# Kernel tuning notes

Measured on AMD Instinct MI355X. Metric: run time of the kernel, lower is better.

Reference implementation:

```python
import jax, jax.numpy as jnp
import numpy as np

B, C, F, D = 128, 16, 128, 512


def setup_inputs() -> dict:
    key = jax.random.key(0)
    k1, k2 = jax.random.split(key)
    return {
        "c_feats": jax.random.normal(k1, (B, C, D), dtype=jnp.float32),
        "f_feats": jax.random.normal(k2, (B, F, D), dtype=jnp.float32),
    }


def _dtw_path_masks(S):
    """S: [P, c, f] per-pair similarity. Returns [P, c, f] 0/1 max-path masks.

    DP: D[i,j] = max(D[i-1,j], D[i,j-1], D[i-1,j-1]) + S[i-1,j-1], D[0,0]=0,
    borders -inf. Tie-break priority (up, left, diag) matches Python max().
    Row recurrence is vectorized: D[i,j] = Csum[j] + cummax_k<=j(A[k]-Csum[k-1])
    where A[k]=max(D[i-1,k], D[i-1,k-1]) (wavefront-free row-parallel form).
    """
    P_, c, f = S.shape
    NEG = -jnp.inf

    init = jnp.concatenate([jnp.zeros((P_, 1), S.dtype),
                            jnp.full((P_, f), NEG, S.dtype)], axis=1)  # D[0, 0..f]

    def row_step(prev, dt_row):
        # prev: [P, f+1] = D[i-1, 0..f]; dt_row: [P, f] = S[i-1, :]
        A = jnp.maximum(prev[:, 1:], prev[:, :-1])                  # max(D[i-1,j], D[i-1,j-1])
        Ccum = jnp.cumsum(dt_row, axis=1)
        Cm1 = jnp.concatenate([jnp.zeros((P_, 1), dt_row.dtype), Ccum[:, :-1]], axis=1)
        row = Ccum + jax.lax.cummax(A - Cm1, axis=1)                # D[i, 1..f]
        new_prev = jnp.concatenate([jnp.full((P_, 1), NEG, dt_row.dtype), row], axis=1)
        return new_prev, new_prev

    _, rows = jax.lax.scan(row_step, init, jnp.moveaxis(S, 1, 0))   # [c, P, f+1]
    Dm = jnp.moveaxis(jnp.concatenate([init[None], rows], axis=0), 1, 0)  # [P, c+1, f+1]

    # Predecessor choice per cell; argmax picks first max -> priority up,left,diag
    up = Dm[:, :-1, 1:]
    left = Dm[:, 1:, :-1]
    diag = Dm[:, :-1, :-1]
    mv = jnp.argmax(jnp.stack([up, left, diag], axis=-1), axis=-1).astype(jnp.int32)
    mv = jnp.pad(mv, ((0, 0), (1, 0), (1, 0)))                      # [P, c+1, f+1]

    pidx = jnp.arange(P_)

    def bt_step(carry, _):
        mask, i, j = carry
        active = (i > 0) | (j > 0)
        mask = mask.at[pidx, i - 1, j - 1].add(jnp.where(active, 1.0, 0.0).astype(mask.dtype))
        m = mv[pidx, i, j]
        di = jnp.where(m == 1, 0, 1)   # left keeps i
        dj = jnp.where(m == 0, 0, 1)   # up keeps j
        i = jnp.where(active, i - di, i)
        j = jnp.where(active, j - dj, j)
        return (mask, i, j), None

    mask0 = jnp.zeros((P_, c, f), jnp.float32)
    i0 = jnp.full((P_,), c, jnp.int32)
    j0 = jnp.full((P_,), f, jnp.int32)
    (mask, _, _), _ = jax.lax.scan(bt_step, (mask0, i0, j0), None, length=c + f)
    return mask


def reference(c_feats, f_feats):
    b, c, d = c_feats.shape
    f = f_feats.shape[1]
    xn = c_feats / jnp.linalg.norm(c_feats, axis=-1, keepdims=True)
    yn = f_feats / jnp.linalg.norm(f_feats, axis=-1, keepdims=True)
    # Source quirk: y row j is normalized only once outer index i reaches it
    # (y[i-1] bug), so S[i,j] uses normalized y[j] iff j <= i, raw y[j] otherwise.
    Sn = jnp.einsum('mcd,nfd->mncf', xn, yn)
    Sr = jnp.einsum('mcd,nfd->mncf', xn, f_feats)
    tri = jnp.arange(f)[None, :] <= jnp.arange(c)[:, None]          # [c, f]: j <= i
    S = jnp.where(tri, Sn, Sr).reshape(b * b, c, f)
    return _dtw_path_masks(S).reshape(b, b, c, f)
```

## Files before the change

kernel.cpp:

```cpp
#include <hip/hip_runtime.h>
#include <stdint.h>

#define M_TOT 2048
#define N_TOT 16384
#define K_TOT 512

typedef _Float16 f16x8 __attribute__((ext_vector_type(8)));
typedef float f32x4 __attribute__((ext_vector_type(4)));
typedef float f32x16 __attribute__((ext_vector_type(16)));

#define AS1 __attribute__((address_space(1)))
#define AS3 __attribute__((address_space(3)))

__device__ __forceinline__ void ld_lds16(const void* g, void* l) {
    __builtin_amdgcn_global_load_lds((const AS1 void*)g, (AS3 void*)l, 16, 0, 0);
}

__device__ __forceinline__ void split4(float x0, float x1, float x2, float x3,
                                       uint2* hs, uint2* ls) {
    union U { _Float16 h[4]; uint2 u; } H, L;
    _Float16 h0 = (_Float16)x0; H.h[0] = h0; L.h[0] = (_Float16)(x0 - (float)h0);
    _Float16 h1 = (_Float16)x1; H.h[1] = h1; L.h[1] = (_Float16)(x1 - (float)h1);
    _Float16 h2 = (_Float16)x2; H.h[2] = h2; L.h[2] = (_Float16)(x2 - (float)h2);
    _Float16 h3 = (_Float16)x3; H.h[3] = h3; L.h[3] = (_Float16)(x3 - (float)h3);
    *hs = H.u; *ls = L.u;
}

__global__ __launch_bounds__(256) void norm_split_kernel(
    const float* __restrict__ c_feats, const float* __restrict__ f_feats,
    _Float16* __restrict__ Ah, _Float16* __restrict__ Al,
    _Float16* __restrict__ Bh, _Float16* __restrict__ Bl,
    float* __restrict__ normf)
{
    int wave = blockIdx.x * 4 + (threadIdx.x >> 6);
    int lane = threadIdx.x & 63;
    if (wave < 2048) {
        const float* row = c_feats + (size_t)wave * K_TOT;
        float4 v0 = ((const float4*)row)[lane];
        float4 v1 = ((const float4*)row)[lane + 64];
        double ss = (double)v0.x * v0.x + (double)v0.y * v0.y +
                    (double)v0.z * v0.z + (double)v0.w * v0.w +
                    (double)v1.x * v1.x + (double)v1.y * v1.y +
                    (double)v1.z * v1.z + (double)v1.w * v1.w;
        #pragma unroll
        for (int off = 32; off; off >>= 1) ss += __shfl_down(ss, off);
        double tot = __shfl(ss, 0);
        float nrm = sqrtf((float)tot);
        float a0 = v0.x / nrm, a1 = v0.y / nrm, a2 = v0.z / nrm, a3 = v0.w / nrm;
        float b0 = v1.x / nrm, b1 = v1.y / nrm, b2 = v1.z / nrm, b3 = v1.w / nrm;
        uint2 h, l;
        split4(a0, a1, a2, a3, &h, &l);
        ((uint2*)(Ah + (size_t)wave * K_TOT))[lane] = h;
        ((uint2*)(Al + (size_t)wave * K_TOT))[lane] = l;
        split4(b0, b1, b2, b3, &h, &l);
        ((uint2*)(Ah + (size_t)wave * K_TOT))[lane + 64] = h;
        ((uint2*)(Al + (size_t)wave * K_TOT))[lane + 64] = l;
    } else if (wave < 18432) {
        int fr = wave - 2048;
        const float* row = f_feats + (size_t)fr * K_TOT;
        float4 v0 = ((const float4*)row)[lane];
        float4 v1 = ((const float4*)row)[lane + 64];
        double ss = (double)v0.x * v0.x + (double)v0.y * v0.y +
                    (double)v0.z * v0.z + (double)v0.w * v0.w +
                    (double)v1.x * v1.x + (double)v1.y * v1.y +
                    (double)v1.z * v1.z + (double)v1.w * v1.w;
        #pragma unroll
        for (int off = 32; off; off >>= 1) ss += __shfl_down(ss, off);
        if (lane == 0) normf[fr] = sqrtf((float)ss);
        uint2 h, l;
        split4(v0.x, v0.y, v0.z, v0.w, &h, &l);
        ((uint2*)(Bh + (size_t)fr * K_TOT))[lane] = h;
        ((uint2*)(Bl + (size_t)fr * K_TOT))[lane] = l;
        split4(v1.x, v1.y, v1.z, v1.w, &h, &l);
        ((uint2*)(Bh + (size_t)fr * K_TOT))[lane + 64] = h;
        ((uint2*)(Bl + (size_t)fr * K_TOT))[lane + 64] = l;
    }
}

__global__ __launch_bounds__(256, 4) void mfma_gemm_kernel(
    const _Float16* __restrict__ Ah, const _Float16* __restrict__ Al,
    const _Float16* __restrict__ Bh, const _Float16* __restrict__ Bl,
    const float* __restrict__ normf,
    float* __restrict__ out)
{
    __shared__ _Float16 sAh[128 * 32];
    __shared__ _Float16 sAl[128 * 32];
    __shared__ _Float16 sBh[128 * 32];
    __shared__ _Float16 sBl[128 * 32];

    const int t = threadIdx.x;
    const int w = t >> 6, lane = t & 63;
    const int ntile = ((blockIdx.x & 7) << 4) | (blockIdx.x >> 3);
    const int gm0 = blockIdx.y * 128, gn0 = ntile * 128;
    const int wm = (w & 1) * 64, wn = (w >> 1) * 64;
    const int m32 = lane & 31;
    const int kql0 = lane >> 5;

    f32x16 acc[2][2] = {};
    const int l0 = w * 128 + lane;

    for (int k0 = 0; k0 < K_TOT; k0 += 32) {
        #pragma unroll
        for (int c = 0; c < 2; ++c) {
            int l = l0 + c * 64;
            int lrow = l >> 2, kq = l & 3;
            int kqs = kq ^ ((lrow >> 1) & 3);
            size_t goffA = (size_t)(gm0 + lrow) * K_TOT + k0 + kqs * 8;
            size_t goffB = (size_t)(gn0 + lrow) * K_TOT + k0 + kqs * 8;
            ld_lds16(Ah + goffA, sAh + (size_t)l * 8);
            ld_lds16(Al + goffA, sAl + (size_t)l * 8);
            ld_lds16(Bh + goffB, sBh + (size_t)l * 8);
            ld_lds16(Bl + goffB, sBl + (size_t)l * 8);
        }
        __syncthreads();

        #pragma unroll
        for (int kh = 0; kh < 2; ++kh) {
            f16x8 fah[2], fal[2], fbh[2], fbl[2];
            #pragma unroll
            for (int x = 0; x < 2; ++x) {
                int arr = wm + x * 32 + m32;
                int brr = wn + x * 32 + m32;
                int kqa = (kh * 2 + kql0) ^ ((arr >> 1) & 3);
                int kqb = (kh * 2 + kql0) ^ ((brr >> 1) & 3);
                int ar = arr * 32 + kqa * 8;
                int br = brr * 32 + kqb * 8;
                fah[x] = *(const f16x8*)(sAh + ar);
                fal[x] = *(const f16x8*)(sAl + ar);
                fbh[x] = *(const f16x8*)(sBh + br);
                fbl[x] = *(const f16x8*)(sBl + br);
            }
            #pragma unroll
            for (int mi = 0; mi < 2; ++mi)
                #pragma unroll
                for (int ni = 0; ni < 2; ++ni) {
                    acc[mi][ni] = __builtin_amdgcn_mfma_f32_32x32x16_f16(fah[mi], fbl[ni], acc[mi][ni], 0, 0, 0);
                    acc[mi][ni] = __builtin_amdgcn_mfma_f32_32x32x16_f16(fal[mi], fbh[ni], acc[mi][ni], 0, 0, 0);
                    acc[mi][ni] = __builtin_amdgcn_mfma_f32_32x32x16_f16(fah[mi], fbh[ni], acc[mi][ni], 0, 0, 0);
                }
        }
        __syncthreads();
    }

    const int nn = ntile;
    const int rq = 4 * (lane >> 5);
    #pragma unroll
    for (int ni = 0; ni < 2; ++ni) {
        int col = wn + ni * 32 + m32;
        bool cn = (col < 16);
        float nf = cn ? normf[gn0 + col] : 1.f;
        #pragma unroll
        for (int mi = 0; mi < 2; ++mi) {
            #pragma unroll
            for (int reg = 0; reg < 16; ++reg) {
                int r = wm + mi * 32 + (reg & 3) + 8 * (reg >> 2) + rq;
                int gm = gm0 + r;
                int mm = gm >> 4, ii = gm & 15;
                float v = acc[mi][ni][reg];
                if (cn && col <= ii) v /= nf;
                out[(((size_t)mm * 128 + nn) * 16 + ii) * 128 + col] = v;
            }
        }
    }
}

#define WQS 304
#define WBUF 1216

__device__ __forceinline__ float dpp_shr1_f32(float x) {
    union { float f; int i; } u, v;
    u.f = x;
    v.i = __builtin_amdgcn_update_dpp(u.i, u.i, 0x111, 0xF, 0xF, false);
    return v.f;
}

__global__ __launch_bounds__(256) void dtw_kernel(float* __restrict__ buf)
{
    __shared__ float swin[4][2 * WBUF];
    __shared__ uint32_t mvw[4][4][132];
    __shared__ int bounds[4][4][16];

    const int lane = threadIdx.x & 63;
    const int w = threadIdx.x >> 6;
    const int q = lane >> 4, r = lane & 15;
    const int pbase = (1023 - blockIdx.x) * 16 + w * 4;
    const float4* gbase = (const float4*)(buf + (size_t)pbase * 2048);
    float* sw = swin[w];
    uint32_t* mvq = &mvw[w][q][0];

    int gidx[4], lidx[4];
    #pragma unroll
    for (int i = 0; i < 4; ++i) {
        gidx[i] = i * 512 + ((lane >> 2) & 15) * 32 + (lane & 3);
        lidx[i] = i * WQS + ((lane >> 2) & 15) * 18 + (lane & 3) * 4;
    }

#define WSTORE(regs, boff)                                                      \
    {                                                                           \
        _Pragma("unroll")                                                       \
        for (int i = 0; i < 4; ++i) {                                           \
            *(float2*)(sw + (boff) + lidx[i])     = make_float2(regs[i].x, regs[i].y); \
            *(float2*)(sw + (boff) + lidx[i] + 2) = make_float2(regs[i].z, regs[i].w); \
        }                                                                       \
    }
#define WLOAD(regs, win)                                                        \
    {                                                                           \
        _Pragma("unroll")                                                       \
        for (int i = 0; i < 4; ++i) regs[i] = gbase[gidx[i] + (win) * 4];       \
    }

    float4 ga[4], gb[4];
    WLOAD(ga, 0)
    WLOAD(gb, 1)
    WSTORE(ga, 0)
    WSTORE(gb, WBUF)
    WLOAD(ga, 2)
    WLOAD(gb, 3)

    const float NEG = -1e30f;
    float Dp = NEG, rawprev = NEG;
    uint32_t mvbuf = 0;
    int j = -r;
    const int sb = q * WQS + r * 18;

#define DTW_STEP(BOUNDARY)                                                      \
    {                                                                           \
        float upr = dpp_shr1_f32(Dp);                                           \
        float dg = rawprev;                                                     \
        rawprev = upr;                                                          \
        float up = (r == 0) ? NEG : upr;                                        \
        float lf = Dp;                                                          \
        if (BOUNDARY) {                                                         \
            if (j == 0) { lf = NEG; dg = (r == 0) ? 0.0f : NEG; }               \
            else if (r == 0) dg = NEG;                                          \
        } else {                                                                \
            if (r == 0) dg = NEG;                                               \
        }                                                                       \
        float sv = sw[(((j >> 4) & 1) ? WBUF : 0) + sb + (j & 15)];             \
        int m = (up >= lf && up >= dg) ? 0 : ((lf >= dg) ? 1 : 2);              \
        float Dc = fmaxf(up, fmaxf(lf, dg)) + sv;                               \
        if ((unsigned)j < 128u) {                                               \
            mvbuf |= (uint32_t)m << (2 * (j & 15));                             \
            if ((j & 15) == 15) { mvq[r * 8 + (j >> 4)] = mvbuf; mvbuf = 0; }   \
        }                                                                       \
        Dp = Dc;                                                                \
        ++j;                                                                    \
    }

    for (int t = 0; t < 16; ++t) DTW_STEP(true)
    for (int t = 16; t < 32; ++t) DTW_STEP(false)
    WSTORE(ga, 0)        WLOAD(ga, 4)
    for (int t = 32; t < 48; ++t) DTW_STEP(false)
    WSTORE(gb, WBUF)     WLOAD(gb, 5)
    for (int t = 48; t < 64; ++t) DTW_STEP(false)
    WSTORE(ga, 0)        WLOAD(ga, 6)
    for (int t = 64; t < 80; ++t) DTW_STEP(false)
    WSTORE(gb, WBUF)     WLOAD(gb, 7)
    for (int t = 80; t < 96; ++t) DTW_STEP(false)
    WSTORE(ga, 0)
    for (int t = 96; t < 112; ++t) DTW_STEP(false)
    WSTORE(gb, WBUF)
    for (int t = 112; t < 143; ++t) DTW_STEP(false)
#undef DTW_STEP
#undef WSTORE
#undef WLOAD

    __syncthreads();

    if (r == 0) {
        int i = 16, jj = 128, hic = 127;
        int cidx = -1;
        uint32_t word = 0;
        for (int it = 0; it < 160; ++it) {
            if (i <= 0) break;
            int idx = (i - 1) * 8 + ((jj - 1) >> 4);
            if (idx != cidx) { word = mvq[idx]; cidx = idx; }
            int m = (int)((word >> (2 * ((jj - 1) & 15))) & 3u);
            if (m == 1) { --jj; continue; }
            bounds[w][q][i - 1] = (jj - 1) | (hic << 8);
            if (m == 2) --jj;
            --i;
            hic = jj - 1;
        }
    }
    __syncthreads();

    #pragma unroll 4
    for (int it = 0; it < 32; ++it) {
        int flat = it * 64 + lane;
        int q2 = flat >> 9;
        int rem = flat & 511;
        int ii = rem >> 5;
        int c4 = rem & 31;
        int b = bounds[w][q2][ii];
        int lo = b & 0xff, hi = (b >> 8) & 0xff;
        int j0 = c4 * 4;
        float4 v;
        v.x = (j0 + 0 >= lo && j0 + 0 <= hi) ? 1.f : 0.f;
        v.y = (j0 + 1 >= lo && j0 + 1 <= hi) ? 1.f : 0.f;
        v.z = (j0 + 2 >= lo && j0 + 2 <= hi) ? 1.f : 0.f;
        v.w = (j0 + 3 >= lo && j0 + 3 <= hi) ? 1.f : 0.f;
        float* tb = buf + (size_t)(pbase + q2) * 2048;
        *(float4*)(tb + ii * 128 + j0) = v;
    }
}

extern "C" void kernel_launch(void* const* d_in, const int* in_sizes, int n_in,
                              void* d_out, int out_size, void* d_ws, size_t ws_size,
                              hipStream_t stream)
{
    const float* c_feats = (const float*)d_in[0];
    const float* f_feats = (const float*)d_in[1];
    float* out = (float*)d_out;

    _Float16* Ah = (_Float16*)d_ws;
    _Float16* Al = Ah + (size_t)M_TOT * K_TOT;
    _Float16* Bh = Al + (size_t)M_TOT * K_TOT;
    _Float16* Bl = Bh + (size_t)N_TOT * K_TOT;
    float* normf = (float*)(Bl + (size_t)N_TOT * K_TOT);

    norm_split_kernel<<<4608, 256, 0, stream>>>(c_feats, f_feats, Ah, Al, Bh, Bl, normf);
    dim3 g(N_TOT / 128, M_TOT / 128);
    mfma_gemm_kernel<<<g, 256, 0, stream>>>(Ah, Al, Bh, Bl, normf, out);
    dtw_kernel<<<1024, 256, 0, stream>>>(out);
}
```

Before: 336.8 us.

## Fuse GEMM and DTW kernels, keeping similarity tiles in LDS

Merges the split-fp16 MFMA GEMM and the DTW path kernel into one kernel. Each 128x128 output tile (8 pairs of 16x128) is written to shared memory instead of global memory, then DTW runs on it in place and only the 0/1 masks go to global. This removes the global write and re-read of the full similarity matrix and one kernel launch. In exchange, half the lanes (q>=2) idle during DTW, LDS use per block rises so occupancy falls (launch bounds drop to 2), and the serial DTW phase now follows the GEMM inside the same block.

```diff
diff --git a/kernel.cpp b/kernel.cpp
--- a/kernel.cpp
+++ b/kernel.cpp
@@ -6,7 +6,6 @@
 #define K_TOT 512
 
 typedef _Float16 f16x8 __attribute__((ext_vector_type(8)));
-typedef float f32x4 __attribute__((ext_vector_type(4)));
 typedef float f32x16 __attribute__((ext_vector_type(16)));
 
 #define AS1 __attribute__((address_space(1)))
@@ -77,16 +76,30 @@
     }
 }
 
-__global__ __launch_bounds__(256, 4) void mfma_gemm_kernel(
+#define SRS 130
+#define SPS 2096
+
+__device__ __forceinline__ float dpp_shr1_f32(float x) {
+    union { float f; int i; } u, v;
+    u.f = x;
+    v.i = __builtin_amdgcn_update_dpp(u.i, u.i, 0x111, 0xF, 0xF, false);
+    return v.f;
+}
+
+__global__ __launch_bounds__(256, 2) void gemm_dtw_kernel(
     const _Float16* __restrict__ Ah, const _Float16* __restrict__ Al,
     const _Float16* __restrict__ Bh, const _Float16* __restrict__ Bl,
     const float* __restrict__ normf,
     float* __restrict__ out)
 {
-    __shared__ _Float16 sAh[128 * 32];
-    __shared__ _Float16 sAl[128 * 32];
-    __shared__ _Float16 sBh[128 * 32];
-    __shared__ _Float16 sBl[128 * 32];
+    __shared__ __attribute__((aligned(16))) float S[8 * SPS];
+    __shared__ uint32_t mv[8][132];
+    __shared__ int bounds[8][16];
+
+    _Float16* const sAh = (_Float16*)S;
+    _Float16* const sAl = sAh + 128 * 32;
+    _Float16* const sBh = sAl + 128 * 32;
+    _Float16* const sBl = sBh + 128 * 32;
 
     const int t = threadIdx.x;
     const int w = t >> 6, lane = t & 63;
@@ -142,86 +155,36 @@
         __syncthreads();
     }
 
-    const int nn = ntile;
-    const int rq = 4 * (lane >> 5);
+    const int rq = 4 * kql0;
     #pragma unroll
     for (int ni = 0; ni < 2; ++ni) {
-        int col = wn + ni * 32 + m32;
-        bool cn = (col < 16);
-        float nf = cn ? normf[gn0 + col] : 1.f;
+        const int col = wn + ni * 32 + m32;
+        const bool cn = (col < 16);
+        const float nf = cn ? normf[gn0 + col] : 1.f;
         #pragma unroll
         for (int mi = 0; mi < 2; ++mi) {
             #pragma unroll
             for (int reg = 0; reg < 16; ++reg) {
-                int r = wm + mi * 32 + (reg & 3) + 8 * (reg >> 2) + rq;
-                int gm = gm0 + r;
-                int mm = gm >> 4, ii = gm & 15;
+                const int rg = wm + mi * 32 + (reg & 3) + 8 * (reg >> 2) + rq;
                 float v = acc[mi][ni][reg];
-                if (cn && col <= ii) v /= nf;
-                out[(((size_t)mm * 128 + nn) * 16 + ii) * 128 + col] = v;
+                if (cn && col <= (rg & 15)) v /= nf;
+                S[(rg >> 4) * SPS + (rg & 15) * SRS + col] = v;
             }
         }
     }
-}
-
-#define WQS 304
-#define WBUF 1216
-
-__device__ __forceinline__ float dpp_shr1_f32(float x) {
-    union { float f; int i; } u, v;
-    u.f = x;
-    v.i = __builtin_amdgcn_update_dpp(u.i, u.i, 0x111, 0xF, 0xF, false);
-    return v.f;
-}
-
-__global__ __launch_bounds__(256) void dtw_kernel(float* __restrict__ buf)
-{
-    __shared__ float swin[4][2 * WBUF];
-    __shared__ uint32_t mvw[4][4][132];
-    __shared__ int bounds[4][4][16];
-
-    const int lane = threadIdx.x & 63;
-    const int w = threadIdx.x >> 6;
+    __syncthreads();
+
     const int q = lane >> 4, r = lane & 15;
-    const int pbase = (1023 - blockIdx.x) * 16 + w * 4;
-    const float4* gbase = (const float4*)(buf + (size_t)pbase * 2048);
-    float* sw = swin[w];
-    uint32_t* mvq = &mvw[w][q][0];
-
-    int gidx[4], lidx[4];
-    #pragma unroll
-    for (int i = 0; i < 4; ++i) {
-        gidx[i] = i * 512 + ((lane >> 2) & 15) * 32 + (lane & 3);
-        lidx[i] = i * WQS + ((lane >> 2) & 15) * 18 + (lane & 3) * 4;
-    }
-
-#define WSTORE(regs, boff)                                                      \
-    {                                                                           \
-        _Pragma("unroll")                                                       \
-        for (int i = 0; i < 4; ++i) {                                           \
-            *(float2*)(sw + (boff) + lidx[i])     = make_float2(regs[i].x, regs[i].y); \
-            *(float2*)(sw + (boff) + lidx[i] + 2) = make_float2(regs[i].z, regs[i].w); \
-        }                                                                       \
-    }
-#define WLOAD(regs, win)                                                        \
-    {                                                                           \
-        _Pragma("unroll")                                                       \
-        for (int i = 0; i < 4; ++i) regs[i] = gbase[gidx[i] + (win) * 4];       \
-    }
-
-    float4 ga[4], gb[4];
-    WLOAD(ga, 0)
-    WLOAD(gb, 1)
-    WSTORE(ga, 0)
-    WSTORE(gb, WBUF)
-    WLOAD(ga, 2)
-    WLOAD(gb, 3)
+    const bool act = (q < 2);
+    const int p = w * 2 + (q & 1);
+    const float* Sp = S + p * SPS + r * SRS;
+    uint32_t* mvq = &mv[p][0];
 
     const float NEG = -1e30f;
     float Dp = NEG, rawprev = NEG;
     uint32_t mvbuf = 0;
     int j = -r;
-    const int sb = q * WQS + r * 18;
+    int svoff = (-r) & 127;
 
 #define DTW_STEP(BOUNDARY)                                                      \
     {                                                                           \
@@ -236,10 +199,11 @@
         } else {                                                                \
             if (r == 0) dg = NEG;                                               \
         }                                                                       \
-        float sv = sw[(((j >> 4) & 1) ? WBUF : 0) + sb + (j & 15)];             \
+        float sv = Sp[svoff];                                                   \
+        svoff = (svoff + 1) & 127;                                              \
         int m = (up >= lf && up >= dg) ? 0 : ((lf >= dg) ? 1 : 2);              \
         float Dc = fmaxf(up, fmaxf(lf, dg)) + sv;                               \
-        if ((unsigned)j < 128u) {                                               \
+        if (act && (unsigned)j < 128u) {                                        \
             mvbuf |= (uint32_t)m << (2 * (j & 15));                             \
             if ((j & 15) == 15) { mvq[r * 8 + (j >> 4)] = mvbuf; mvbuf = 0; }   \
         }                                                                       \
@@ -247,27 +211,13 @@
         ++j;                                                                    \
     }
 
-    for (int t = 0; t < 16; ++t) DTW_STEP(true)
-    for (int t = 16; t < 32; ++t) DTW_STEP(false)
-    WSTORE(ga, 0)        WLOAD(ga, 4)
-    for (int t = 32; t < 48; ++t) DTW_STEP(false)
-    WSTORE(gb, WBUF)     WLOAD(gb, 5)
-    for (int t = 48; t < 64; ++t) DTW_STEP(false)
-    WSTORE(ga, 0)        WLOAD(ga, 6)
-    for (int t = 64; t < 80; ++t) DTW_STEP(false)
-    WSTORE(gb, WBUF)     WLOAD(gb, 7)
-    for (int t = 80; t < 96; ++t) DTW_STEP(false)
-    WSTORE(ga, 0)
-    for (int t = 96; t < 112; ++t) DTW_STEP(false)
-    WSTORE(gb, WBUF)
-    for (int t = 112; t < 143; ++t) DTW_STEP(false)
+    #pragma unroll
+    for (int tt = 0; tt < 16; ++tt) DTW_STEP(true)
+    #pragma unroll
+    for (int tt = 16; tt < 143; ++tt) DTW_STEP(false)
 #undef DTW_STEP
-#undef WSTORE
-#undef WLOAD
-
-    __syncthreads();
-
-    if (r == 0) {
+
+    if (r == 0 && act) {
         int i = 16, jj = 128, hic = 127;
         int cidx = -1;
         uint32_t word = 0;
@@ -277,22 +227,23 @@
             if (idx != cidx) { word = mvq[idx]; cidx = idx; }
             int m = (int)((word >> (2 * ((jj - 1) & 15))) & 3u);
             if (m == 1) { --jj; continue; }
-            bounds[w][q][i - 1] = (jj - 1) | (hic << 8);
+            bounds[p][i - 1] = (jj - 1) | (hic << 8);
             if (m == 2) --jj;
             --i;
             hic = jj - 1;
         }
     }
-    __syncthreads();
-
+
+    const int nn = ntile;
+    const int mmb = gm0 >> 4;
     #pragma unroll 4
-    for (int it = 0; it < 32; ++it) {
+    for (int it = 0; it < 16; ++it) {
         int flat = it * 64 + lane;
         int q2 = flat >> 9;
         int rem = flat & 511;
         int ii = rem >> 5;
         int c4 = rem & 31;
-        int b = bounds[w][q2][ii];
+        int b = bounds[w * 2 + q2][ii];
         int lo = b & 0xff, hi = (b >> 8) & 0xff;
         int j0 = c4 * 4;
         float4 v;
@@ -300,7 +251,7 @@
         v.y = (j0 + 1 >= lo && j0 + 1 <= hi) ? 1.f : 0.f;
         v.z = (j0 + 2 >= lo && j0 + 2 <= hi) ? 1.f : 0.f;
         v.w = (j0 + 3 >= lo && j0 + 3 <= hi) ? 1.f : 0.f;
-        float* tb = buf + (size_t)(pbase + q2) * 2048;
+        float* tb = out + ((size_t)((mmb + w * 2 + q2) * 128 + nn)) * 2048;
         *(float4*)(tb + ii * 128 + j0) = v;
     }
 }
@@ -321,6 +272,5 @@
 
     norm_split_kernel<<<4608, 256, 0, stream>>>(c_feats, f_feats, Ah, Al, Bh, Bl, normf);
     dim3 g(N_TOT / 128, M_TOT / 128);
-    mfma_gemm_kernel<<<g, 256, 0, stream>>>(Ah, Al, Bh, Bl, normf, out);
-    dtw_kernel<<<1024, 256, 0, stream>>>(out);
-}
+    gemm_dtw_kernel<<<g, 256, 0, stream>>>(Ah, Al, Bh, Bl, normf, out);
+}
```

Result: slower. 370.8 us (+10.1%).
